# Kernel tuning notes

Measured on AMD Instinct MI355X. Metric: run time of the kernel, lower is better.

The kernel has to match this reference:

```python
import jax, jax.numpy as jnp
import numpy as np

D_MODEL = 1024
H = 16
DK = D_MODEL // H
D_FC = 4096
B = 2
S = 1024
EPS = 1e-6


def setup_inputs() -> dict:
    key = jax.random.key(0)
    ks = jax.random.split(key, 8)
    sc = 1.0 / np.sqrt(D_MODEL)
    return {
        "x": jax.random.normal(ks[0], (B, S, D_MODEL), dtype=jnp.float32),
        "mask": jnp.ones((B, 1, 1, S), dtype=jnp.int32),
        "w_q": jax.random.normal(ks[1], (D_MODEL, D_MODEL), dtype=jnp.float32) * sc,
        "w_k": jax.random.normal(ks[2], (D_MODEL, D_MODEL), dtype=jnp.float32) * sc,
        "w_v": jax.random.normal(ks[3], (D_MODEL, D_MODEL), dtype=jnp.float32) * sc,
        "w_o": jax.random.normal(ks[4], (D_MODEL, D_MODEL), dtype=jnp.float32) * sc,
        "alpha1": jnp.ones((D_MODEL,), dtype=jnp.float32),
        "beta1": jnp.zeros((D_MODEL,), dtype=jnp.float32),
        "alpha2": jnp.ones((D_MODEL,), dtype=jnp.float32),
        "beta2": jnp.zeros((D_MODEL,), dtype=jnp.float32),
        "fc1_w": jax.random.normal(ks[5], (D_FC, D_MODEL), dtype=jnp.float32) * sc,
        "fc1_b": jnp.zeros((D_FC,), dtype=jnp.float32),
        "fc2_w": jax.random.normal(ks[6], (D_MODEL, D_FC), dtype=jnp.float32) * (1.0 / np.sqrt(D_FC)),
        "fc2_b": jnp.zeros((D_MODEL,), dtype=jnp.float32),
    }


def _layernorm(x, alpha, beta):
    # Matches torch: mean and std (unbiased, ddof=1), divide by (std + eps)
    mean = jnp.mean(x, axis=-1, keepdims=True)
    std = jnp.std(x, axis=-1, keepdims=True, ddof=1)
    return alpha * (x - mean) / (std + EPS) + beta


def _mha(x, mask, w_q, w_k, w_v, w_o):
    # nn.Linear(bias=False): y = x @ W.T
    q = (x @ w_q.T).reshape(B, S, H, DK).transpose(0, 2, 1, 3)  # (B,H,S,DK)
    k = (x @ w_k.T).reshape(B, S, H, DK).transpose(0, 2, 1, 3)
    v = (x @ w_v.T).reshape(B, S, H, DK).transpose(0, 2, 1, 3)
    scores = jnp.einsum('bhqd,bhkd->bhqk', q, k) / jnp.sqrt(jnp.float32(DK))
    scores = jnp.where(mask == 0, jnp.float32(-1e9), scores)
    attn = jax.nn.softmax(scores, axis=-1)  # dropout=0 (eval)
    out = jnp.einsum('bhqk,bhkd->bhqd', attn, v)  # (B,H,S,DK)
    out = out.transpose(0, 2, 1, 3).reshape(B, S, D_MODEL)
    return out @ w_o.T


def _ffn(x, fc1_w, fc1_b, fc2_w, fc2_b):
    h = jax.nn.relu(x @ fc1_w.T + fc1_b)
    return h @ fc2_w.T + fc2_b


def reference(x, mask, w_q, w_k, w_v, w_o, alpha1, beta1, alpha2, beta2,
              fc1_w, fc1_b, fc2_w, fc2_b):
    # Pre-LN residual block 1: attention
    x = x + _mha(_layernorm(x, alpha1, beta1), mask, w_q, w_k, w_v, w_o)
    # Pre-LN residual block 2: FFN
    x = x + _ffn(_layernorm(x, alpha2, beta2), fc1_w, fc1_b, fc2_w, fc2_b)
    return x
```

## Files before the change

kernel.cpp:

```cpp
#include <hip/hip_runtime.h>
#include <hip/hip_bf16.h>


typedef __bf16 bf16;
typedef __attribute__((ext_vector_type(8))) __bf16 bf16x8;
typedef __attribute__((ext_vector_type(4))) __bf16 bf16x4;
typedef __attribute__((ext_vector_type(4))) float f32x4;

#define NTOK 2048
#define DM   1024
#define DFC  4096
#define QKVN 3072

__device__ inline void gl_lds16(const void* g, void* l) {
    __builtin_amdgcn_global_load_lds((const __attribute__((address_space(1))) void*)g,
                                     (__attribute__((address_space(3))) void*)l, 16, 0, 0);
}

__device__ inline void ln_row(float4 v, const float* alpha, const float* beta,
                              bf16* outrow, int t) {
    float s  = v.x + v.y + v.z + v.w;
    float ss = v.x * v.x + v.y * v.y + v.z * v.z + v.w * v.w;
    __shared__ float red[8];
    int lane = t & 63, wv = t >> 6;
    #pragma unroll
    for (int o = 32; o > 0; o >>= 1) {
        s  += __shfl_down(s, o);
        ss += __shfl_down(ss, o);
    }
    if (lane == 0) { red[wv] = s; red[4 + wv] = ss; }
    __syncthreads();
    float S  = red[0] + red[1] + red[2] + red[3];
    float SS = red[4] + red[5] + red[6] + red[7];
    float mean = S * (1.0f / 1024.0f);
    float var  = (SS - S * mean) * (1.0f / 1023.0f);
    var = var < 0.f ? 0.f : var;
    float inv = 1.0f / (sqrtf(var) + 1e-6f);
    float4 a4 = reinterpret_cast<const float4*>(alpha)[t];
    float4 b4 = reinterpret_cast<const float4*>(beta)[t];
    bf16x4 o4;
    o4[0] = (bf16)(a4.x * (v.x - mean) * inv + b4.x);
    o4[1] = (bf16)(a4.y * (v.y - mean) * inv + b4.y);
    o4[2] = (bf16)(a4.z * (v.z - mean) * inv + b4.z);
    o4[3] = (bf16)(a4.w * (v.w - mean) * inv + b4.w);
    reinterpret_cast<bf16x4*>(outrow)[t] = o4;
}

__global__ __launch_bounds__(256) void prep_kernel(
    const float4* __restrict__ wq, const float4* __restrict__ wk,
    const float4* __restrict__ wv, const float4* __restrict__ wo,
    const float4* __restrict__ f1, const float4* __restrict__ f2,
    bf16x4* __restrict__ oqkv, bf16x4* __restrict__ oo,
    bf16x4* __restrict__ of1, bf16x4* __restrict__ of2,
    const float* __restrict__ x, const float* __restrict__ alpha1,
    const float* __restrict__ beta1, bf16* __restrict__ xn) {
    int blk = blockIdx.x;
    int t = threadIdx.x;
    if (blk < 12288) {
        int i = blk * 256 + t;
        const int Q = 262144;
        float4 v;
        bf16x4* dst;
        if (i < 3 * Q) {
            v = (i < Q) ? wq[i] : (i < 2 * Q) ? wk[i - Q] : wv[i - 2 * Q];
            dst = oqkv + i;
        } else if (i < 4 * Q) {
            v = wo[i - 3 * Q];
            dst = oo + (i - 3 * Q);
        } else if (i < 8 * Q) {
            v = f1[i - 4 * Q];
            dst = of1 + (i - 4 * Q);
        } else {
            v = f2[i - 8 * Q];
            dst = of2 + (i - 8 * Q);
        }
        bf16x4 o;
        o[0] = (bf16)v.x; o[1] = (bf16)v.y; o[2] = (bf16)v.z; o[3] = (bf16)v.w;
        *dst = o;
    } else {
        int row = blk - 12288;
        float4 v = reinterpret_cast<const float4*>(x + (size_t)row * DM)[t];
        ln_row(v, alpha1, beta1, xn + (size_t)row * DM, t);
    }
}

__global__ __launch_bounds__(256) void reduce_ln_kernel(const float* __restrict__ p,
                                                        const float* __restrict__ resid,
                                                        const float* __restrict__ alpha,
                                                        const float* __restrict__ beta,
                                                        float* __restrict__ x2,
                                                        bf16* __restrict__ xn) {
    int row = blockIdx.x, t = threadIdx.x;
    size_t i4 = (size_t)row * 256 + t;
    float4 a = reinterpret_cast<const float4*>(p)[i4];
    float4 b = reinterpret_cast<const float4*>(p)[i4 + 524288];
    float4 r = reinterpret_cast<const float4*>(resid)[i4];
    float4 v;
    v.x = a.x + b.x + r.x; v.y = a.y + b.y + r.y;
    v.z = a.z + b.z + r.z; v.w = a.w + b.w + r.w;
    reinterpret_cast<float4*>(x2)[i4] = v;
    ln_row(v, alpha, beta, xn + (size_t)row * DM, t);
}

__global__ __launch_bounds__(256) void reduce_out_kernel(const float* __restrict__ p,
                                                         const float* __restrict__ bias,
                                                         const float* __restrict__ x2,
                                                         float* __restrict__ out) {
    size_t i4 = (size_t)blockIdx.x * 256 + threadIdx.x;
    float4 a = reinterpret_cast<const float4*>(p)[i4];
    float4 b = reinterpret_cast<const float4*>(p)[i4 + 524288];
    float4 r = reinterpret_cast<const float4*>(x2)[i4];
    float4 bi = reinterpret_cast<const float4*>(bias)[i4 & 255];
    float4 o;
    o.x = a.x + b.x + r.x + bi.x; o.y = a.y + b.y + r.y + bi.y;
    o.z = a.z + b.z + r.z + bi.z; o.w = a.w + b.w + r.w + bi.w;
    reinterpret_cast<float4*>(out)[i4] = o;
}

template <int EPI>
__global__ __launch_bounds__(256) void gemm128(const bf16* __restrict__ A,
                                               const bf16* __restrict__ Bt,
                                               void* __restrict__ outp,
                                               const float* __restrict__ bias,
                                               int M, int N, int K, int kslice) {
    __shared__ bf16 As[2][128 * 64];
    __shared__ bf16 Bs[2][128 * 64];
    int tid = threadIdx.x;
    int lane = tid & 63, wave = tid >> 6;
    int q = lane >> 4, r = lane & 15;
    int wm = wave >> 1, wn = wave & 1;

    int lid = blockIdx.y * gridDim.x + blockIdx.x;
    int nxp = gridDim.x >> 3;
    int xcd = lid & 7;
    int loc = lid >> 3;
    int bx = xcd * nxp + (loc % nxp);
    int by = loc / nxp;

    int m0 = by * 128, n0 = bx * 128;
    int kbeg = blockIdx.z * kslice;
    int nit = kslice / 64;
    f32x4 acc[4][4] = {};

    int srow = tid >> 3;
    int csrc = (tid & 7) ^ (srow & 7);
    const bf16* agp = A  + (size_t)(m0 + srow) * K + kbeg + csrc * 8;
    const bf16* bgp = Bt + (size_t)(n0 + srow) * K + kbeg + csrc * 8;

    int rsw = (r & 7);
    int co0 = ((q ^ rsw) * 8);
    int co1 = co0 ^ 32;
    int aoff = (wm * 64 + r) * 64;
    int boff = (wn * 64 + r) * 64;

    auto stage = [&](int it, int b) {
        int k0 = it * 64;
        #pragma unroll
        for (int j = 0; j < 4; ++j) {
            gl_lds16(agp + (size_t)j * 32 * K + k0, &As[b][tid * 8 + j * 2048]);
            gl_lds16(bgp + (size_t)j * 32 * K + k0, &Bs[b][tid * 8 + j * 2048]);
        }
    };

    stage(0, 0);
    for (int it = 0; it < nit; ++it) {
        __syncthreads();
        if (it + 1 < nit) stage(it + 1, (it + 1) & 1);
        const bf16* Ab = &As[it & 1][aoff];
        const bf16* Bb = &Bs[it & 1][boff];
        #pragma unroll
        for (int half = 0; half < 2; ++half) {
            int co = half ? co1 : co0;
            bf16x8 af[4], bfv[4];
            #pragma unroll
            for (int t = 0; t < 4; ++t)
                af[t] = *reinterpret_cast<const bf16x8*>(Ab + t * 1024 + co);
            #pragma unroll
            for (int u = 0; u < 4; ++u)
                bfv[u] = *reinterpret_cast<const bf16x8*>(Bb + u * 1024 + co);
            #pragma unroll
            for (int t = 0; t < 4; ++t)
                #pragma unroll
                for (int u = 0; u < 4; ++u)
                    acc[t][u] = __builtin_amdgcn_mfma_f32_16x16x32_bf16(af[t], bfv[u], acc[t][u], 0, 0, 0);
        }
    }

    size_t zoff = (size_t)blockIdx.z * M * N;
    #pragma unroll
    for (int t = 0; t < 4; ++t) {
        #pragma unroll
        for (int u = 0; u < 4; ++u) {
            #pragma unroll
            for (int i = 0; i < 4; ++i) {
                int mm = m0 + wm * 64 + t * 16 + q * 4 + i;
                int nn = n0 + wn * 64 + u * 16 + r;
                size_t idx = (size_t)mm * N + nn;
                float v = acc[t][u][i];
                if (EPI == 0) {
                    ((bf16*)outp)[idx] = (bf16)v;
                } else if (EPI == 1) {
                    v += bias[nn];
                    ((bf16*)outp)[idx] = (bf16)(v > 0.f ? v : 0.f);
                } else {
                    ((float*)outp)[zoff + idx] = v;
                }
            }
        }
    }
}

__global__ void transpose_v(const bf16* __restrict__ qkv, bf16* __restrict__ vt) {
    __shared__ bf16 tile[32][33];
    int bh = blockIdx.z;
    int b = bh >> 4, h = bh & 15;
    int s0 = blockIdx.x * 32;
    int d0 = blockIdx.y * 32;
    int tx = threadIdx.x, ty = threadIdx.y;
    tile[ty][tx] = qkv[(size_t)(b * 1024 + s0 + ty) * QKVN + 2048 + h * 64 + d0 + tx];
    __syncthreads();
    vt[(size_t)(bh * 64 + d0 + ty) * 1024 + s0 + tx] = tile[tx][ty];
}

__global__ __launch_bounds__(256) void attn_kernel(const bf16* __restrict__ qkv,
                                                   const bf16* __restrict__ Vt,
                                                   const int* __restrict__ mask,
                                                   bf16* __restrict__ out) {
    __shared__ bf16 Ks[2][4096];
    __shared__ bf16 Vs[2][4096];
    __shared__ bf16 pbuf[4][1024];
    __shared__ float msk[1024];
    int tid = threadIdx.x;
    int lane = tid & 63, w = tid >> 6;
    int q = lane >> 4, r = lane & 15;

    int id = blockIdx.x;
    int xcd = id & 7, j = id >> 3;
    int bh = xcd * 4 + (j >> 4);
    int qb = j & 15;
    int b = bh >> 4, h = bh & 15;

    {
        int4 mi = reinterpret_cast<const int4*>(mask + b * 1024)[tid];
        msk[tid * 4 + 0] = mi.x ? 0.f : -1e9f;
        msk[tid * 4 + 1] = mi.y ? 0.f : -1e9f;
        msk[tid * 4 + 2] = mi.z ? 0.f : -1e9f;
        msk[tid * 4 + 3] = mi.w ? 0.f : -1e9f;
    }

    const bf16* qrow = qkv + (size_t)(b * 1024 + qb * 64 + w * 16 + r) * QKVN + h * 64 + q * 8;
    bf16x8 qf0 = *reinterpret_cast<const bf16x8*>(qrow);
    bf16x8 qf1 = *reinterpret_cast<const bf16x8*>(qrow + 32);

    int csw = (tid & 7) ^ ((tid >> 3) & 7);
    const bf16* kg0 = qkv + (size_t)(b * 1024 + (tid >> 3)) * QKVN + 1024 + h * 64 + csw * 8;
    const bf16* kg1 = kg0 + (size_t)32 * QKVN;
    const bf16* vg0 = Vt + (size_t)((b * 16 + h) * 64 + (tid >> 3)) * 1024 + csw * 8;
    const bf16* vg1 = vg0 + 32 * 1024;
    bf16* kld = &Ks[0][tid * 8];
    bf16* vld = &Vs[0][tid * 8];

    int co0 = (q ^ (r & 7)) * 8;
    bf16* pw = pbuf[w];
    bf16x8 ones;
    #pragma unroll
    for (int jj = 0; jj < 8; ++jj) ones[jj] = (bf16)1.0f;

    float m[4] = {-1e30f, -1e30f, -1e30f, -1e30f};
    f32x4 osum = {};
    f32x4 o[4] = {};

    gl_lds16(kg0, kld);
    gl_lds16(kg1, kld + 2048);
    gl_lds16(vg0, vld);
    gl_lds16(vg1, vld + 2048);

    for (int t = 0; t < 16; ++t) {
        __syncthreads();
        if (t < 15) {
            int ktn = (t + 1) * 64;
            int bo = ((t + 1) & 1) * 4096;
            gl_lds16(kg0 + (size_t)ktn * QKVN, kld + bo);
            gl_lds16(kg1 + (size_t)ktn * QKVN, kld + bo + 2048);
            gl_lds16(vg0 + ktn, vld + bo);
            gl_lds16(vg1 + ktn, vld + bo + 2048);
        }
        const bf16* Kb = Ks[t & 1];
        const bf16* Vb = Vs[t & 1];
        int kt = t * 64;

        f32x4 s[4];
        #pragma unroll
        for (int ks = 0; ks < 4; ++ks) {
            bf16x8 kf0 = *reinterpret_cast<const bf16x8*>(&Kb[(ks * 16 + r) * 64 + co0]);
            bf16x8 kf1 = *reinterpret_cast<const bf16x8*>(&Kb[(ks * 16 + r) * 64 + (co0 ^ 32)]);
            f32x4 a = {};
            a = __builtin_amdgcn_mfma_f32_16x16x32_bf16(qf0, kf0, a, 0, 0, 0);
            a = __builtin_amdgcn_mfma_f32_16x16x32_bf16(qf1, kf1, a, 0, 0, 0);
            float mb = msk[kt + ks * 16 + r];
            #pragma unroll
            for (int i = 0; i < 4; ++i) s[ks][i] = fmaf(a[i], 0.125f, mb);
        }
        float alpha[4];
        #pragma unroll
        for (int i = 0; i < 4; ++i) {
            float t2 = fmaxf(fmaxf(s[0][i], s[1][i]), fmaxf(s[2][i], s[3][i]));
            t2 = fmaxf(t2, __shfl_xor(t2, 1));
            t2 = fmaxf(t2, __shfl_xor(t2, 2));
            t2 = fmaxf(t2, __shfl_xor(t2, 4));
            t2 = fmaxf(t2, __shfl_xor(t2, 8));
            float mn = fmaxf(m[i], t2);
            alpha[i] = __expf(m[i] - mn);
            m[i] = mn;
        }
        #pragma unroll
        for (int i = 0; i < 4; ++i) {
            s[0][i] = __expf(s[0][i] - m[i]);
            s[1][i] = __expf(s[1][i] - m[i]);
            s[2][i] = __expf(s[2][i] - m[i]);
            s[3][i] = __expf(s[3][i] - m[i]);
        }
        #pragma unroll
        for (int i = 0; i < 4; ++i) {
            osum[i] *= alpha[i];
            o[0][i] *= alpha[i]; o[1][i] *= alpha[i];
            o[2][i] *= alpha[i]; o[3][i] *= alpha[i];
        }
        #pragma unroll
        for (int ks = 0; ks < 4; ++ks) {
            int kc = ks * 2 + (r >> 3);
            #pragma unroll
            for (int i = 0; i < 4; ++i) {
                int mr = q * 4 + i;
                pw[mr * 64 + ((kc ^ (mr & 7)) * 8) + (r & 7)] = (bf16)s[ks][i];
            }
        }
        #pragma unroll
        for (int ks2 = 0; ks2 < 2; ++ks2) {
            int vpo = (((ks2 * 4 + q) ^ (r & 7)) * 8);
            bf16x8 pf = *reinterpret_cast<const bf16x8*>(&pw[r * 64 + vpo]);
            #pragma unroll
            for (int nt = 0; nt < 4; ++nt) {
                bf16x8 vf = *reinterpret_cast<const bf16x8*>(&Vb[(nt * 16 + r) * 64 + vpo]);
                o[nt] = __builtin_amdgcn_mfma_f32_16x16x32_bf16(pf, vf, o[nt], 0, 0, 0);
            }
            osum = __builtin_amdgcn_mfma_f32_16x16x32_bf16(pf, ones, osum, 0, 0, 0);
        }
    }

    float inv[4];
    #pragma unroll
    for (int i = 0; i < 4; ++i) inv[i] = 1.0f / osum[i];
    #pragma unroll
    for (int nt = 0; nt < 4; ++nt)
        #pragma unroll
        for (int i = 0; i < 4; ++i)
            out[(size_t)(b * 1024 + qb * 64 + w * 16 + q * 4 + i) * DM + h * 64 + nt * 16 + r] =
                (bf16)(o[nt][i] * inv[i]);
}

extern "C" void kernel_launch(void* const* d_in, const int* in_sizes, int n_in,
                              void* d_out, int out_size, void* d_ws, size_t ws_size,
                              hipStream_t stream) {
    const float* x      = (const float*)d_in[0];
    const int*   mask   = (const int*)  d_in[1];
    const float* w_q    = (const float*)d_in[2];
    const float* w_k    = (const float*)d_in[3];
    const float* w_v    = (const float*)d_in[4];
    const float* w_o    = (const float*)d_in[5];
    const float* alpha1 = (const float*)d_in[6];
    const float* beta1  = (const float*)d_in[7];
    const float* alpha2 = (const float*)d_in[8];
    const float* beta2  = (const float*)d_in[9];
    const float* fc1_w  = (const float*)d_in[10];
    const float* fc1_b  = (const float*)d_in[11];
    const float* fc2_w  = (const float*)d_in[12];
    const float* fc2_b  = (const float*)d_in[13];
    float* out = (float*)d_out;

    char* ws = (char*)d_ws;
    const size_t MB = 1024 * 1024;
    bf16*  wqkv_b = (bf16*)(ws +  0 * MB);
    bf16*  wo_b   = (bf16*)(ws +  6 * MB);
    bf16*  f1w_b  = (bf16*)(ws +  8 * MB);
    bf16*  f2w_b  = (bf16*)(ws + 16 * MB);
    bf16*  xn     = (bf16*)(ws + 24 * MB);
    bf16*  qkvb   = (bf16*)(ws + 28 * MB);
    bf16*  vtb    = (bf16*)(ws + 40 * MB);
    bf16*  attnb  = (bf16*)(ws + 44 * MB);
    float* x2     = (float*)(ws + 48 * MB);
    float* po     = (float*)(ws + 28 * MB);
    bf16*  hb     = (bf16*)(ws + 28 * MB);
    float* pf2    = (float*)(ws +  0 * MB);

    prep_kernel<<<14336, 256, 0, stream>>>(
        (const float4*)w_q, (const float4*)w_k, (const float4*)w_v, (const float4*)w_o,
        (const float4*)fc1_w, (const float4*)fc2_w,
        (bf16x4*)wqkv_b, (bf16x4*)wo_b, (bf16x4*)f1w_b, (bf16x4*)f2w_b,
        x, alpha1, beta1, xn);

    gemm128<0><<<dim3(QKVN / 128, NTOK / 128, 1), 256, 0, stream>>>(
        xn, wqkv_b, qkvb, nullptr, NTOK, QKVN, DM, DM);

    transpose_v<<<dim3(32, 2, 32), dim3(32, 32), 0, stream>>>(qkvb, vtb);

    attn_kernel<<<512, 256, 0, stream>>>(qkvb, vtb, mask, attnb);

    gemm128<4><<<dim3(DM / 128, NTOK / 128, 2), 256, 0, stream>>>(
        attnb, wo_b, po, nullptr, NTOK, DM, DM, DM / 2);

    reduce_ln_kernel<<<NTOK, 256, 0, stream>>>(po, x, alpha2, beta2, x2, xn);

    gemm128<1><<<dim3(DFC / 128, NTOK / 128, 1), 256, 0, stream>>>(
        xn, f1w_b, hb, fc1_b, NTOK, DFC, DM, DM);

    gemm128<4><<<dim3(DM / 128, NTOK / 128, 2), 256, 0, stream>>>(
        hb, f2w_b, pf2, nullptr, NTOK, DM, DFC, DFC / 2);

    reduce_out_kernel<<<2048, 256, 0, stream>>>(pf2, fc2_b, x2, out);
}
```

Measured before the change: 260.4 us.

## Fuse V transpose into QKV GEMM epilogue and raise split-K to four

The QKV GEMM gets a new epilogue that writes V columns straight into the transposed Vt layout, which removes the separate transpose_v kernel and its extra global round trip. The Wo and FC2 GEMMs now split K four ways instead of two, giving 512 blocks per launch for better CU occupancy, and the reduce kernels sum four partials. Workspace buffers are moved so the larger partial arrays no longer alias live data. The transposed V stores from the epilogue are strided and uncoalesced, and the larger split-K adds fp32 partial traffic.

```diff
diff --git a/kernel.cpp b/kernel.cpp
--- a/kernel.cpp
+++ b/kernel.cpp
@@ -92,12 +92,17 @@
                                                         bf16* __restrict__ xn) {
     int row = blockIdx.x, t = threadIdx.x;
     size_t i4 = (size_t)row * 256 + t;
+    const size_t SL = 524288;
     float4 a = reinterpret_cast<const float4*>(p)[i4];
-    float4 b = reinterpret_cast<const float4*>(p)[i4 + 524288];
+    float4 b = reinterpret_cast<const float4*>(p)[i4 + SL];
+    float4 c = reinterpret_cast<const float4*>(p)[i4 + 2 * SL];
+    float4 d = reinterpret_cast<const float4*>(p)[i4 + 3 * SL];
     float4 r = reinterpret_cast<const float4*>(resid)[i4];
     float4 v;
-    v.x = a.x + b.x + r.x; v.y = a.y + b.y + r.y;
-    v.z = a.z + b.z + r.z; v.w = a.w + b.w + r.w;
+    v.x = (a.x + b.x) + (c.x + d.x) + r.x;
+    v.y = (a.y + b.y) + (c.y + d.y) + r.y;
+    v.z = (a.z + b.z) + (c.z + d.z) + r.z;
+    v.w = (a.w + b.w) + (c.w + d.w) + r.w;
     reinterpret_cast<float4*>(x2)[i4] = v;
     ln_row(v, alpha, beta, xn + (size_t)row * DM, t);
 }
@@ -107,13 +112,18 @@
                                                          const float* __restrict__ x2,
                                                          float* __restrict__ out) {
     size_t i4 = (size_t)blockIdx.x * 256 + threadIdx.x;
+    const size_t SL = 524288;
     float4 a = reinterpret_cast<const float4*>(p)[i4];
-    float4 b = reinterpret_cast<const float4*>(p)[i4 + 524288];
+    float4 b = reinterpret_cast<const float4*>(p)[i4 + SL];
+    float4 c = reinterpret_cast<const float4*>(p)[i4 + 2 * SL];
+    float4 d = reinterpret_cast<const float4*>(p)[i4 + 3 * SL];
     float4 r = reinterpret_cast<const float4*>(x2)[i4];
     float4 bi = reinterpret_cast<const float4*>(bias)[i4 & 255];
     float4 o;
-    o.x = a.x + b.x + r.x + bi.x; o.y = a.y + b.y + r.y + bi.y;
-    o.z = a.z + b.z + r.z + bi.z; o.w = a.w + b.w + r.w + bi.w;
+    o.x = (a.x + b.x) + (c.x + d.x) + r.x + bi.x;
+    o.y = (a.y + b.y) + (c.y + d.y) + r.y + bi.y;
+    o.z = (a.z + b.z) + (c.z + d.z) + r.z + bi.z;
+    o.w = (a.w + b.w) + (c.w + d.w) + r.w + bi.w;
     reinterpret_cast<float4*>(out)[i4] = o;
 }
 
@@ -121,6 +131,7 @@
 __global__ __launch_bounds__(256) void gemm128(const bf16* __restrict__ A,
                                                const bf16* __restrict__ Bt,
                                                void* __restrict__ outp,
+                                               void* __restrict__ outp2,
                                                const float* __restrict__ bias,
                                                int M, int N, int K, int kslice) {
     __shared__ bf16 As[2][128 * 64];
@@ -134,8 +145,13 @@
     int nxp = gridDim.x >> 3;
     int xcd = lid & 7;
     int loc = lid >> 3;
-    int bx = xcd * nxp + (loc % nxp);
-    int by = loc / nxp;
+    int bx, by;
+    if (nxp > 0) {
+        bx = xcd * nxp + (loc % nxp);
+        by = loc / nxp;
+    } else {
+        bx = blockIdx.x; by = blockIdx.y;
+    }
 
     int m0 = by * 128, n0 = bx * 128;
     int kbeg = blockIdx.z * kslice;
@@ -202,24 +218,19 @@
                 } else if (EPI == 1) {
                     v += bias[nn];
                     ((bf16*)outp)[idx] = (bf16)(v > 0.f ? v : 0.f);
+                } else if (EPI == 5) {
+                    if (nn < 2048) {
+                        ((bf16*)outp)[idx] = (bf16)v;
+                    } else {
+                        size_t tidx = ((size_t)((mm >> 10) * 1024 + (nn - 2048))) * 1024 + (mm & 1023);
+                        ((bf16*)outp2)[tidx] = (bf16)v;
+                    }
                 } else {
                     ((float*)outp)[zoff + idx] = v;
                 }
             }
         }
     }
-}
-
-__global__ void transpose_v(const bf16* __restrict__ qkv, bf16* __restrict__ vt) {
-    __shared__ bf16 tile[32][33];
-    int bh = blockIdx.z;
-    int b = bh >> 4, h = bh & 15;
-    int s0 = blockIdx.x * 32;
-    int d0 = blockIdx.y * 32;
-    int tx = threadIdx.x, ty = threadIdx.y;
-    tile[ty][tx] = qkv[(size_t)(b * 1024 + s0 + ty) * QKVN + 2048 + h * 64 + d0 + tx];
-    __syncthreads();
-    vt[(size_t)(bh * 64 + d0 + ty) * 1024 + s0 + tx] = tile[tx][ty];
 }
 
 __global__ __launch_bounds__(256) void attn_kernel(const bf16* __restrict__ qkv,
@@ -380,18 +391,18 @@
 
     char* ws = (char*)d_ws;
     const size_t MB = 1024 * 1024;
-    bf16*  wqkv_b = (bf16*)(ws +  0 * MB);
-    bf16*  wo_b   = (bf16*)(ws +  6 * MB);
-    bf16*  f1w_b  = (bf16*)(ws +  8 * MB);
-    bf16*  f2w_b  = (bf16*)(ws + 16 * MB);
-    bf16*  xn     = (bf16*)(ws + 24 * MB);
-    bf16*  qkvb   = (bf16*)(ws + 28 * MB);
-    bf16*  vtb    = (bf16*)(ws + 40 * MB);
-    bf16*  attnb  = (bf16*)(ws + 44 * MB);
-    float* x2     = (float*)(ws + 48 * MB);
-    float* po     = (float*)(ws + 28 * MB);
-    bf16*  hb     = (bf16*)(ws + 28 * MB);
-    float* pf2    = (float*)(ws +  0 * MB);
+    bf16*  wqkv_b = (bf16*)(ws +   0 * MB);
+    bf16*  wo_b   = (bf16*)(ws +   6 * MB);
+    bf16*  f1w_b  = (bf16*)(ws +   8 * MB);
+    bf16*  f2w_b  = (bf16*)(ws +  16 * MB);
+    bf16*  xn     = (bf16*)(ws +  24 * MB);
+    bf16*  qkvb   = (bf16*)(ws +  28 * MB);
+    bf16*  vtb    = (bf16*)(ws +  40 * MB);
+    bf16*  attnb  = (bf16*)(ws +  44 * MB);
+    float* x2     = (float*)(ws +  48 * MB);
+    float* po     = (float*)(ws +  64 * MB);
+    bf16*  hb     = (bf16*)(ws +  96 * MB);
+    float* pf2    = (float*)(ws + 112 * MB);
 
     prep_kernel<<<14336, 256, 0, stream>>>(
         (const float4*)w_q, (const float4*)w_k, (const float4*)w_v, (const float4*)w_o,
@@ -399,23 +410,21 @@
         (bf16x4*)wqkv_b, (bf16x4*)wo_b, (bf16x4*)f1w_b, (bf16x4*)f2w_b,
         x, alpha1, beta1, xn);
 
-    gemm128<0><<<dim3(QKVN / 128, NTOK / 128, 1), 256, 0, stream>>>(
-        xn, wqkv_b, qkvb, nullptr, NTOK, QKVN, DM, DM);
-
-    transpose_v<<<dim3(32, 2, 32), dim3(32, 32), 0, stream>>>(qkvb, vtb);
+    gemm128<5><<<dim3(QKVN / 128, NTOK / 128, 1), 256, 0, stream>>>(
+        xn, wqkv_b, qkvb, vtb, nullptr, NTOK, QKVN, DM, DM);
 
     attn_kernel<<<512, 256, 0, stream>>>(qkvb, vtb, mask, attnb);
 
-    gemm128<4><<<dim3(DM / 128, NTOK / 128, 2), 256, 0, stream>>>(
-        attnb, wo_b, po, nullptr, NTOK, DM, DM, DM / 2);
+    gemm128<4><<<dim3(DM / 128, NTOK / 128, 4), 256, 0, stream>>>(
+        attnb, wo_b, po, nullptr, nullptr, NTOK, DM, DM, DM / 4);
 
     reduce_ln_kernel<<<NTOK, 256, 0, stream>>>(po, x, alpha2, beta2, x2, xn);
 
     gemm128<1><<<dim3(DFC / 128, NTOK / 128, 1), 256, 0, stream>>>(
-        xn, f1w_b, hb, fc1_b, NTOK, DFC, DM, DM);
-
-    gemm128<4><<<dim3(DM / 128, NTOK / 128, 2), 256, 0, stream>>>(
-        hb, f2w_b, pf2, nullptr, NTOK, DM, DFC, DFC / 2);
+        xn, f1w_b, hb, nullptr, fc1_b, NTOK, DFC, DM, DM);
+
+    gemm128<4><<<dim3(DM / 128, NTOK / 128, 4), 256, 0, stream>>>(
+        hb, f2w_b, pf2, nullptr, nullptr, NTOK, DM, DFC, DFC / 4);
 
     reduce_out_kernel<<<2048, 256, 0, stream>>>(pf2, fc2_b, x2, out);
 }
```

After: 261.6 us. No clear change (+0.5%).
